# Optimization experiments

Hardware: AMD Instinct MI355X
Metric: run time of the kernel (lower is better)

## Reference

```python
import jax, jax.numpy as jnp
import numpy as np

B = 64        # graphs per batch
N = 2048      # nodes per graph
BN = B * N
BE = BN * 16  # edges (avg degree 16)
C1 = 64
C2 = 64
M = 16
K_EDGES = 4   # hardcoded k=4 in original forward


def setup_inputs() -> dict:
    key = jax.random.key(0)
    k1, k2, k3, k4, k5, k6 = jax.random.split(key, 6)
    x = jax.random.normal(k1, (BN, C1), dtype=jnp.float32)
    e_ = jax.random.randint(k2, (2, BE), 0, BN, dtype=jnp.int32)
    b_ = jnp.repeat(jnp.arange(B, dtype=jnp.int32), N)  # sorted batch index
    # Linear params (stored as (in, out); torch stores (out, in))
    W_assign = jax.random.normal(k3, (C1, M), dtype=jnp.float32) / np.sqrt(C1)
    b_assign = jax.random.normal(k4, (M,), dtype=jnp.float32) * 0.01
    W_embed = jax.random.normal(k5, (C1, C2 - 3), dtype=jnp.float32) / np.sqrt(C1)
    b_embed = jax.random.normal(k6, (C2 - 3,), dtype=jnp.float32) * 0.01
    return {"x": x, "e_": e_, "b_": b_, "W_assign": W_assign,
            "b_assign": b_assign, "W_embed": W_embed, "b_embed": b_embed}


def reference(x, e_, b_, W_assign, b_assign, W_embed, b_embed):
    BN_, _ = x.shape
    Bn = int(jnp.max(b_)) + 1
    Mm = W_assign.shape[1]

    p = x[:, :3]                                   # (BN, 3) positions
    f = x @ W_embed + b_embed                      # (BN, C2-3)
    S = jax.nn.softmax(x @ W_assign + b_assign, axis=-1)  # (BN, M)

    # Weighted scatter-reduce pooling: index_add over (batch*M + m)
    # == per-batch segment_sum of S[n,m] * feat[n,c]
    Zf = jax.ops.segment_sum(S[:, :, None] * f[:, None, :], b_, num_segments=Bn)  # (B, M, C2-3)
    Zp = jax.ops.segment_sum(S[:, :, None] * p[:, None, :], b_, num_segments=Bn)  # (B, M, 3)
    w = jax.ops.segment_sum(S, b_, num_segments=Bn)                               # (B, M)
    w = jnp.maximum(w, 1e-10)
    Zp = Zp / w[..., None]
    x_out = jnp.concatenate([Zp, Zf], axis=-1).reshape(Bn * Mm, -1)  # (B*M, C2)

    # Sparse adjacency pooling: AS = A_NN @ S (A_NN[src,dst]=1 per edge)
    AS = jax.ops.segment_sum(S[e_[1]], e_[0], num_segments=BN_)  # (BN, M)
    # A_MM[b] = (S^T masked to batch b) @ AS
    A_MM = jax.ops.segment_sum(S[:, :, None] * AS[:, None, :], b_, num_segments=Bn)  # (B, M, M)

    # top-k edge construction on pooled adjacency
    dst = jax.lax.top_k(A_MM, K_EDGES)[1]                                # (B, M, k)
    src = jnp.broadcast_to(jnp.arange(Mm)[None, :, None], (Bn, Mm, K_EDGES))
    offset = (jnp.arange(Bn) * Mm)[:, None, None]
    e_out = jnp.stack([(src + offset).reshape(-1), (dst + offset).reshape(-1)], axis=0)
    b_out = jnp.repeat(jnp.arange(Bn), Mm)
    return x_out, e_out, b_out
```

## Files before the change

### kernel.cpp

```cpp
#include <hip/hip_runtime.h>

#define BN 131072
#define BE 2097152
#define NGR 64
#define CAP 36864

#define XS_OFF     0
#define WACC_OFF   262144
#define A_OFF      266240
#define ZERO_U4    20736
#define CUR_OFF    331776
#define QS_OFF     332032
#define ENDS_OFF   333056
#define SH_OFF     2430208
#define PK_OFF     6624512

__global__ __launch_bounds__(256) void k_zero(uint4* __restrict__ zbase,
                                              int* __restrict__ cur)
{
    int zi = blockIdx.x * 256 + threadIdx.x;
    if (zi < ZERO_U4) zbase[zi] = make_uint4(0u, 0u, 0u, 0u);
    if (blockIdx.x == 0 && threadIdx.x < NGR) cur[threadIdx.x] = threadIdx.x * CAP;
}

__global__ __launch_bounds__(256) void k_scatterS(const int* __restrict__ e_,
                                                  int* __restrict__ cur,
                                                  unsigned* __restrict__ packed)
{
    __shared__ int h[64];
    __shared__ int gb[64];
    int t = threadIdx.x;
    if (t < 64) h[t] = 0;
    __syncthreads();
    size_t base = (size_t)blockIdx.x * 4096;
    int e0v[16], e1v[16], rk[16];
    #pragma unroll
    for (int k = 0; k < 16; ++k) {
        size_t i = base + k * 256 + t;
        e0v[k] = e_[i];
        e1v[k] = e_[BE + i];
        rk[k] = atomicAdd(&h[e0v[k] >> 11], 1);
    }
    __syncthreads();
    if (t < 64) gb[t] = atomicAdd(&cur[t], h[t]);
    __syncthreads();
    #pragma unroll
    for (int k = 0; k < 16; ++k) {
        int b = e0v[k] >> 11;
        packed[gb[b] + rk[k]] = ((unsigned)(e0v[k] & 2047) << 17) | (unsigned)e1v[k];
    }
}

__global__ __launch_bounds__(128) void k_node(const float* __restrict__ x,
                                              const float* __restrict__ Wa,
                                              const float* __restrict__ ba,
                                              unsigned short* __restrict__ Sh,
                                              float* __restrict__ Xs,
                                              float* __restrict__ wacc)
{
    __shared__ __align__(16) float Xl[128 * 65];
    __shared__ __align__(16) float Sl[128 * 20];
    __shared__ float Wl[64 * 16];

    const int t = threadIdx.x;
    const int blk = blockIdx.x;
    const int g = blk >> 4;

    const float4* xg4 = (const float4*)(x + (size_t)blk * 128 * 64);
    #pragma unroll
    for (int it = 0; it < 16; ++it) {
        int idx4 = it * 128 + t;
        float4 v = xg4[idx4];
        int node = idx4 >> 4;
        int c4 = (idx4 & 15) * 4;
        float* p = &Xl[node * 65 + c4];
        p[0] = v.x; p[1] = v.y; p[2] = v.z; p[3] = v.w;
    }
    for (int i = t; i < 1024; i += 128) Wl[i] = Wa[i];
    __syncthreads();

    float lg[16];
    #pragma unroll
    for (int m = 0; m < 16; ++m) lg[m] = ba[m];
    for (int c = 0; c < 64; ++c) {
        float xc = Xl[t * 65 + c];
        #pragma unroll
        for (int m = 0; m < 16; ++m) lg[m] += xc * Wl[c * 16 + m];
    }
    float mx = lg[0];
    #pragma unroll
    for (int m = 1; m < 16; ++m) mx = fmaxf(mx, lg[m]);
    float s[16]; float sum = 0.f;
    #pragma unroll
    for (int m = 0; m < 16; ++m) { s[m] = expf(lg[m] - mx); sum += s[m]; }
    float inv = 1.f / sum;
    #pragma unroll
    for (int m = 0; m < 16; ++m) s[m] *= inv;

    const size_t node = (size_t)blk * 128 + t;
    #pragma unroll
    for (int q = 0; q < 4; ++q) {
        float4 v4 = make_float4(s[q*4], s[q*4+1], s[q*4+2], s[q*4+3]);
        *(float4*)(&Sl[t * 20 + q * 4]) = v4;
    }
    {
        unsigned pk8[8];
        #pragma unroll
        for (int j = 0; j < 8; ++j) {
            unsigned b0 = __float_as_uint(s[2*j]);
            unsigned b1 = __float_as_uint(s[2*j+1]);
            unsigned h0 = (b0 + 0x7FFFu + ((b0 >> 16) & 1u)) >> 16;
            unsigned h1 = (b1 + 0x7FFFu + ((b1 >> 16) & 1u)) >> 16;
            pk8[j] = h0 | (h1 << 16);
        }
        uint4* hrow = (uint4*)(Sh + node * 16);
        hrow[0] = make_uint4(pk8[0], pk8[1], pk8[2], pk8[3]);
        hrow[1] = make_uint4(pk8[4], pk8[5], pk8[6], pk8[7]);
    }
    __syncthreads();

    const int c = t & 63;
    const int half = t >> 6;
    float acc[8];
    #pragma unroll
    for (int j = 0; j < 8; ++j) acc[j] = 0.f;
    for (int n = 0; n < 128; ++n) {
        float xv = Xl[n * 65 + c];
        float4 sa = *(const float4*)(&Sl[n * 20 + half * 8]);
        float4 sb = *(const float4*)(&Sl[n * 20 + half * 8 + 4]);
        acc[0] += sa.x * xv; acc[1] += sa.y * xv; acc[2] += sa.z * xv; acc[3] += sa.w * xv;
        acc[4] += sb.x * xv; acc[5] += sb.y * xv; acc[6] += sb.z * xv; acc[7] += sb.w * xv;
    }
    float* xsg = Xs + g * 1024;
    #pragma unroll
    for (int j = 0; j < 8; ++j) atomicAdd(&xsg[(half * 8 + j) * 64 + c], acc[j]);

    if (t < 16) {
        float ws_ = 0.f;
        for (int n = 0; n < 128; ++n) ws_ += Sl[n * 20 + t];
        atomicAdd(&wacc[g * 16 + t], ws_);
    }
}

#define SBUF_CAP 9216
__global__ __launch_bounds__(256) void k_sortL(unsigned* __restrict__ packed,
                                               const int* __restrict__ cur,
                                               int* __restrict__ qs,
                                               int* __restrict__ ends4)
{
    __shared__ unsigned sbuf[SBUF_CAP];
    __shared__ unsigned sout[SBUF_CAP];
    __shared__ int h[2048];
    __shared__ int psum[256];
    const int t = threadIdx.x;
    const int Q = blockIdx.x;
    const int g = Q >> 2;
    const int q = Q & 3;
    const int slab = g * CAP;
    const int n = cur[g] - slab;
    const int chunk = (n + 3) >> 2;
    const int qlo = slab + min(q * chunk, n);
    const int qhi = slab + min((q + 1) * chunk, n);
    const int nq = qhi - qlo;
    if (t == 0) qs[Q] = qlo;

    for (int i = t; i < 2048; i += 256) h[i] = 0;
    __syncthreads();
    for (int i = t; i < nq; i += 256) {
        unsigned u = packed[qlo + i];
        sbuf[i] = u;
        atomicAdd(&h[u >> 17], 1);
    }
    __syncthreads();

    int hl[8]; int s = 0;
    #pragma unroll
    for (int j = 0; j < 8; ++j) { hl[j] = h[t * 8 + j]; s += hl[j]; }
    psum[t] = s;
    __syncthreads();
    for (int off = 1; off < 256; off <<= 1) {
        int v = (t >= off) ? psum[t - off] : 0;
        __syncthreads();
        psum[t] += v;
        __syncthreads();
    }
    int run = psum[t] - s;
    int* ends = ends4 + (Q << 11);
    #pragma unroll
    for (int j = 0; j < 8; ++j) {
        int bin = t * 8 + j;
        int c = hl[j];
        h[bin] = run;
        run += c;
        ends[bin] = qlo + run;
    }
    __syncthreads();
    for (int i = t; i < nq; i += 256) {
        unsigned u = sbuf[i];
        int pos = atomicAdd(&h[u >> 17], 1);
        sout[pos] = u & 131071u;
    }
    __syncthreads();
    for (int i = t; i < nq; i += 256) packed[qlo + i] = sout[i];
}

__global__ __launch_bounds__(256) void k_edge(const unsigned* __restrict__ se1,
                                              const unsigned short* __restrict__ Sh,
                                              const int* __restrict__ ends4,
                                              const int* __restrict__ qs,
                                              float* __restrict__ A)
{
    __shared__ __align__(16) float ASl[64 * 16];
    const int t = threadIdx.x;
    const int blk = blockIdx.x;
    const int g = blk >> 5;
    const int nbase = blk << 6;

    {
        const int qd = t >> 2;
        const int c4 = (t & 3) << 2;
        const int nl = (nbase & 2047) + qd;
        const unsigned short* __restrict__ ShB = Sh + c4;
        float a0 = 0.f, a1 = 0.f, a2 = 0.f, a3 = 0.f;
        float b0 = 0.f, b1 = 0.f, b2 = 0.f, b3 = 0.f;
        #pragma unroll
        for (int q = 0; q < 4; ++q) {
            const int Qb = (g << 2) + q;
            const int* __restrict__ ends = ends4 + (Qb << 11);
            int lo = nl ? ends[nl - 1] : qs[Qb];
            int hi = ends[nl];
            int i = lo;
            for (; i + 2 <= hi; i += 2) {
                unsigned ea = se1[i];
                unsigned eb = se1[i + 1];
                uint2 ra = *(const uint2*)(ShB + ((size_t)ea << 4));
                uint2 rb = *(const uint2*)(ShB + ((size_t)eb << 4));
                a0 += __uint_as_float(ra.x << 16);
                a1 += __uint_as_float(ra.x & 0xFFFF0000u);
                a2 += __uint_as_float(ra.y << 16);
                a3 += __uint_as_float(ra.y & 0xFFFF0000u);
                b0 += __uint_as_float(rb.x << 16);
                b1 += __uint_as_float(rb.x & 0xFFFF0000u);
                b2 += __uint_as_float(rb.y << 16);
                b3 += __uint_as_float(rb.y & 0xFFFF0000u);
            }
            if (i < hi) {
                unsigned ea = se1[i];
                uint2 ra = *(const uint2*)(ShB + ((size_t)ea << 4));
                a0 += __uint_as_float(ra.x << 16);
                a1 += __uint_as_float(ra.x & 0xFFFF0000u);
                a2 += __uint_as_float(ra.y << 16);
                a3 += __uint_as_float(ra.y & 0xFFFF0000u);
            }
        }
        *(float4*)(&ASl[qd * 16 + c4]) = make_float4(a0 + b0, a1 + b1, a2 + b2, a3 + b3);
    }
    __syncthreads();

    {
        const int m = t >> 4;
        const int k = t & 15;
        const unsigned short* __restrict__ SgM = Sh + ((size_t)nbase << 4) + m;
        float a = 0.f;
        #pragma unroll 4
        for (int i = 0; i < 64; ++i) {
            float sv = __uint_as_float((unsigned)SgM[(size_t)i << 4] << 16);
            a += sv * ASl[i * 16 + k];
        }
        atomicAdd(&A[(g << 8) + t], a);
    }
}

__global__ __launch_bounds__(256) void k_xt(const float* __restrict__ Xs,
                                            const float* __restrict__ wacc,
                                            const float* __restrict__ We,
                                            const float* __restrict__ be,
                                            const float* __restrict__ A,
                                            float* __restrict__ out)
{
    const int t = threadIdx.x;
    const int blk = blockIdx.x;
    if (blk < 256) {
        int lane = t & 63;
        int row = blk * 4 + (t >> 6);
        const float* xs = Xs + row * 64;
        float w = wacc[row];
        float val;
        if (lane < 3) {
            val = xs[lane] / fmaxf(w, 1e-10f);
        } else {
            int c2 = lane - 3;
            float accv = w * be[c2];
            for (int cc = 0; cc < 64; ++cc) accv += xs[cc] * We[cc * 61 + c2];
            val = accv;
        }
        out[row * 64 + lane] = val;
    } else {
        int r = (blk - 256) * 256 + t;
        float v[16];
        #pragma unroll
        for (int i = 0; i < 16; ++i) v[i] = A[r * 16 + i];
        float* e0o = out + 65536;
        float* e1o = out + 65536 + 4096;
        float* bo  = out + 65536 + 8192;
        unsigned mask = 0;
        #pragma unroll
        for (int rep = 0; rep < 4; ++rep) {
            float best = -3.4e38f; int bi = 0;
            #pragma unroll
            for (int i = 0; i < 16; ++i) {
                bool ok = (((mask >> i) & 1u) == 0u) && (v[i] > best);
                if (ok) { best = v[i]; bi = i; }
            }
            mask |= (1u << bi);
            e0o[r * 4 + rep] = (float)r;
            e1o[r * 4 + rep] = (float)((r & ~15) + bi);
        }
        bo[r] = (float)(r >> 4);
    }
}

extern "C" void kernel_launch(void* const* d_in, const int* in_sizes, int n_in,
                              void* d_out, int out_size, void* d_ws, size_t ws_size,
                              hipStream_t stream)
{
    const float* x  = (const float*)d_in[0];
    const int*   e  = (const int*)d_in[1];
    const float* Wa = (const float*)d_in[3];
    const float* ba = (const float*)d_in[4];
    const float* We = (const float*)d_in[5];
    const float* be = (const float*)d_in[6];

    char* ws = (char*)d_ws;
    float* Xs     = (float*)(ws + XS_OFF);
    float* wacc   = (float*)(ws + WACC_OFF);
    float* A      = (float*)(ws + A_OFF);
    int*   cur    = (int*)(ws + CUR_OFF);
    int*   qs     = (int*)(ws + QS_OFF);
    int*   ends4  = (int*)(ws + ENDS_OFF);
    unsigned short* Sh = (unsigned short*)(ws + SH_OFF);
    unsigned* packed = (unsigned*)(ws + PK_OFF);

    k_zero    <<<82, 256, 0, stream>>>((uint4*)ws, cur);
    k_scatterS<<<512, 256, 0, stream>>>(e, cur, packed);
    k_node    <<<1024, 128, 0, stream>>>(x, Wa, ba, Sh, Xs, wacc);
    k_sortL   <<<256, 256, 0, stream>>>(packed, cur, qs, ends4);
    k_edge    <<<2048, 256, 0, stream>>>(packed, Sh, ends4, qs, A);
    k_xt      <<<260, 256, 0, stream>>>(Xs, wacc, We, be, A, (float*)d_out);
}
```

Baseline: 104.5 us.

## Fuse edge scatter with node pass and sort with edge aggregation

Edge bucketing and the per-node softmax/pooling kernel are merged into one launch, with block index selecting the role. The local counting sort and the edge gather/A_MM accumulation are also merged, so sorted edge lists stay in shared memory. This removes the global sorted-edge write-back, the ends/qs arrays and two launches. In exchange, all gather work now runs in 256 blocks that loop over 32 node chunks with barriers, instead of 2048 independent blocks, which lowers parallelism for a latency-bound gather.

```diff
diff --git a/kernel.cpp b/kernel.cpp
--- a/kernel.cpp
+++ b/kernel.cpp
@@ -10,10 +10,11 @@
 #define A_OFF      266240
 #define ZERO_U4    20736
 #define CUR_OFF    331776
-#define QS_OFF     332032
-#define ENDS_OFF   333056
-#define SH_OFF     2430208
-#define PK_OFF     6624512
+#define SH_OFF     332032
+#define PK_OFF     4526336
+
+__device__ __forceinline__ float bflo(unsigned u) { return __uint_as_float(u << 16); }
+__device__ __forceinline__ float bfhi(unsigned u) { return __uint_as_float(u & 0xFFFF0000u); }
 
 __global__ __launch_bounds__(256) void k_zero(uint4* __restrict__ zbase,
                                               int* __restrict__ cur)
@@ -23,50 +24,52 @@
     if (blockIdx.x == 0 && threadIdx.x < NGR) cur[threadIdx.x] = threadIdx.x * CAP;
 }
 
-__global__ __launch_bounds__(256) void k_scatterS(const int* __restrict__ e_,
+__global__ __launch_bounds__(128) void k_scatNode(const int* __restrict__ e_,
                                                   int* __restrict__ cur,
-                                                  unsigned* __restrict__ packed)
-{
-    __shared__ int h[64];
-    __shared__ int gb[64];
-    int t = threadIdx.x;
-    if (t < 64) h[t] = 0;
-    __syncthreads();
-    size_t base = (size_t)blockIdx.x * 4096;
-    int e0v[16], e1v[16], rk[16];
-    #pragma unroll
-    for (int k = 0; k < 16; ++k) {
-        size_t i = base + k * 256 + t;
-        e0v[k] = e_[i];
-        e1v[k] = e_[BE + i];
-        rk[k] = atomicAdd(&h[e0v[k] >> 11], 1);
-    }
-    __syncthreads();
-    if (t < 64) gb[t] = atomicAdd(&cur[t], h[t]);
-    __syncthreads();
-    #pragma unroll
-    for (int k = 0; k < 16; ++k) {
-        int b = e0v[k] >> 11;
-        packed[gb[b] + rk[k]] = ((unsigned)(e0v[k] & 2047) << 17) | (unsigned)e1v[k];
-    }
-}
-
-__global__ __launch_bounds__(128) void k_node(const float* __restrict__ x,
-                                              const float* __restrict__ Wa,
-                                              const float* __restrict__ ba,
-                                              unsigned short* __restrict__ Sh,
-                                              float* __restrict__ Xs,
-                                              float* __restrict__ wacc)
-{
-    __shared__ __align__(16) float Xl[128 * 65];
-    __shared__ __align__(16) float Sl[128 * 20];
-    __shared__ float Wl[64 * 16];
-
+                                                  unsigned* __restrict__ packed,
+                                                  const float* __restrict__ x,
+                                                  const float* __restrict__ Wa,
+                                                  const float* __restrict__ ba,
+                                                  unsigned short* __restrict__ Sh,
+                                                  float* __restrict__ Xs,
+                                                  float* __restrict__ wacc)
+{
+    __shared__ __align__(16) unsigned char smem[47616];
     const int t = threadIdx.x;
     const int blk = blockIdx.x;
-    const int g = blk >> 4;
-
-    const float4* xg4 = (const float4*)(x + (size_t)blk * 128 * 64);
+
+    if (blk < 1024) {
+        int* h  = (int*)smem;
+        int* gb = (int*)(smem + 256);
+        if (t < 64) h[t] = 0;
+        __syncthreads();
+        size_t base = (size_t)blk * 2048;
+        int e0v[16], e1v[16], rk[16];
+        #pragma unroll
+        for (int k = 0; k < 16; ++k) {
+            size_t i = base + k * 128 + t;
+            e0v[k] = e_[i];
+            e1v[k] = e_[BE + i];
+            rk[k] = atomicAdd(&h[e0v[k] >> 11], 1);
+        }
+        __syncthreads();
+        if (t < 64) gb[t] = atomicAdd(&cur[t], h[t]);
+        __syncthreads();
+        #pragma unroll
+        for (int k = 0; k < 16; ++k) {
+            int b = e0v[k] >> 11;
+            packed[gb[b] + rk[k]] = ((unsigned)(e0v[k] & 2047) << 17) | (unsigned)e1v[k];
+        }
+        return;
+    }
+
+    const int nblk = blk - 1024;
+    const int g = nblk >> 4;
+    float* Xl = (float*)smem;
+    float* Sl = (float*)(smem + 33280);
+    float* Wl = (float*)(smem + 43520);
+
+    const float4* xg4 = (const float4*)(x + (size_t)nblk * 128 * 64);
     #pragma unroll
     for (int it = 0; it < 16; ++it) {
         int idx4 = it * 128 + t;
@@ -97,7 +100,7 @@
     #pragma unroll
     for (int m = 0; m < 16; ++m) s[m] *= inv;
 
-    const size_t node = (size_t)blk * 128 + t;
+    const size_t node = (size_t)nblk * 128 + t;
     #pragma unroll
     for (int q = 0; q < 4; ++q) {
         float4 v4 = make_float4(s[q*4], s[q*4+1], s[q*4+2], s[q*4+3]);
@@ -142,16 +145,16 @@
     }
 }
 
-#define SBUF_CAP 9216
-__global__ __launch_bounds__(256) void k_sortL(unsigned* __restrict__ packed,
-                                               const int* __restrict__ cur,
-                                               int* __restrict__ qs,
-                                               int* __restrict__ ends4)
-{
-    __shared__ unsigned sbuf[SBUF_CAP];
-    __shared__ unsigned sout[SBUF_CAP];
+#define SE_CAP 9216
+__global__ __launch_bounds__(256) void k_sortEdge(const unsigned* __restrict__ packed,
+                                                  const int* __restrict__ cur,
+                                                  const unsigned short* __restrict__ Sh,
+                                                  float* __restrict__ A)
+{
+    __shared__ unsigned sout[SE_CAP];
     __shared__ int h[2048];
     __shared__ int psum[256];
+    __shared__ __align__(16) float ASl[64 * 16];
     const int t = threadIdx.x;
     const int Q = blockIdx.x;
     const int g = Q >> 2;
@@ -162,13 +165,11 @@
     const int qlo = slab + min(q * chunk, n);
     const int qhi = slab + min((q + 1) * chunk, n);
     const int nq = qhi - qlo;
-    if (t == 0) qs[Q] = qlo;
 
     for (int i = t; i < 2048; i += 256) h[i] = 0;
     __syncthreads();
     for (int i = t; i < nq; i += 256) {
         unsigned u = packed[qlo + i];
-        sbuf[i] = u;
         atomicAdd(&h[u >> 17], 1);
     }
     __syncthreads();
@@ -185,90 +186,60 @@
         __syncthreads();
     }
     int run = psum[t] - s;
-    int* ends = ends4 + (Q << 11);
     #pragma unroll
     for (int j = 0; j < 8; ++j) {
-        int bin = t * 8 + j;
-        int c = hl[j];
-        h[bin] = run;
-        run += c;
-        ends[bin] = qlo + run;
-    }
-    __syncthreads();
+        h[t * 8 + j] = run;
+        run += hl[j];
+    }
+    __syncthreads();
+
     for (int i = t; i < nq; i += 256) {
-        unsigned u = sbuf[i];
+        unsigned u = packed[qlo + i];
         int pos = atomicAdd(&h[u >> 17], 1);
         sout[pos] = u & 131071u;
     }
     __syncthreads();
-    for (int i = t; i < nq; i += 256) packed[qlo + i] = sout[i];
-}
-
-__global__ __launch_bounds__(256) void k_edge(const unsigned* __restrict__ se1,
-                                              const unsigned short* __restrict__ Sh,
-                                              const int* __restrict__ ends4,
-                                              const int* __restrict__ qs,
-                                              float* __restrict__ A)
-{
-    __shared__ __align__(16) float ASl[64 * 16];
-    const int t = threadIdx.x;
-    const int blk = blockIdx.x;
-    const int g = blk >> 5;
-    const int nbase = blk << 6;
-
-    {
-        const int qd = t >> 2;
-        const int c4 = (t & 3) << 2;
-        const int nl = (nbase & 2047) + qd;
-        const unsigned short* __restrict__ ShB = Sh + c4;
+
+    const int qd = t >> 2;
+    const int c4 = (t & 3) << 2;
+    const unsigned short* __restrict__ ShB = Sh + c4;
+    const int m = t >> 4;
+    const int k = t & 15;
+    const unsigned short* __restrict__ SgM = Sh + (((size_t)g << 11) << 4) + m;
+    float aacc = 0.f;
+
+    for (int ch = 0; ch < 32; ++ch) {
+        const int nl = (ch << 6) + qd;
+        int lo = nl ? h[nl - 1] : 0;
+        int hi = h[nl];
         float a0 = 0.f, a1 = 0.f, a2 = 0.f, a3 = 0.f;
         float b0 = 0.f, b1 = 0.f, b2 = 0.f, b3 = 0.f;
-        #pragma unroll
-        for (int q = 0; q < 4; ++q) {
-            const int Qb = (g << 2) + q;
-            const int* __restrict__ ends = ends4 + (Qb << 11);
-            int lo = nl ? ends[nl - 1] : qs[Qb];
-            int hi = ends[nl];
-            int i = lo;
-            for (; i + 2 <= hi; i += 2) {
-                unsigned ea = se1[i];
-                unsigned eb = se1[i + 1];
-                uint2 ra = *(const uint2*)(ShB + ((size_t)ea << 4));
-                uint2 rb = *(const uint2*)(ShB + ((size_t)eb << 4));
-                a0 += __uint_as_float(ra.x << 16);
-                a1 += __uint_as_float(ra.x & 0xFFFF0000u);
-                a2 += __uint_as_float(ra.y << 16);
-                a3 += __uint_as_float(ra.y & 0xFFFF0000u);
-                b0 += __uint_as_float(rb.x << 16);
-                b1 += __uint_as_float(rb.x & 0xFFFF0000u);
-                b2 += __uint_as_float(rb.y << 16);
-                b3 += __uint_as_float(rb.y & 0xFFFF0000u);
-            }
-            if (i < hi) {
-                unsigned ea = se1[i];
-                uint2 ra = *(const uint2*)(ShB + ((size_t)ea << 4));
-                a0 += __uint_as_float(ra.x << 16);
-                a1 += __uint_as_float(ra.x & 0xFFFF0000u);
-                a2 += __uint_as_float(ra.y << 16);
-                a3 += __uint_as_float(ra.y & 0xFFFF0000u);
-            }
+        int i = lo;
+        for (; i + 2 <= hi; i += 2) {
+            unsigned ea = sout[i];
+            unsigned eb = sout[i + 1];
+            uint2 ra = *(const uint2*)(ShB + ((size_t)ea << 4));
+            uint2 rb = *(const uint2*)(ShB + ((size_t)eb << 4));
+            a0 += bflo(ra.x); a1 += bfhi(ra.x); a2 += bflo(ra.y); a3 += bfhi(ra.y);
+            b0 += bflo(rb.x); b1 += bfhi(rb.x); b2 += bflo(rb.y); b3 += bfhi(rb.y);
+        }
+        if (i < hi) {
+            unsigned ea = sout[i];
+            uint2 ra = *(const uint2*)(ShB + ((size_t)ea << 4));
+            a0 += bflo(ra.x); a1 += bfhi(ra.x); a2 += bflo(ra.y); a3 += bfhi(ra.y);
         }
         *(float4*)(&ASl[qd * 16 + c4]) = make_float4(a0 + b0, a1 + b1, a2 + b2, a3 + b3);
-    }
-    __syncthreads();
-
-    {
-        const int m = t >> 4;
-        const int k = t & 15;
-        const unsigned short* __restrict__ SgM = Sh + ((size_t)nbase << 4) + m;
-        float a = 0.f;
+        __syncthreads();
+
+        const int nb = ch << 6;
         #pragma unroll 4
-        for (int i = 0; i < 64; ++i) {
-            float sv = __uint_as_float((unsigned)SgM[(size_t)i << 4] << 16);
-            a += sv * ASl[i * 16 + k];
-        }
-        atomicAdd(&A[(g << 8) + t], a);
-    }
+        for (int i2 = 0; i2 < 64; ++i2) {
+            float sv = __uint_as_float((unsigned)SgM[(size_t)(nb + i2) << 4] << 16);
+            aacc += sv * ASl[i2 * 16 + k];
+        }
+        __syncthreads();
+    }
+    atomicAdd(&A[(g << 8) + t], aacc);
 }
 
 __global__ __launch_bounds__(256) void k_xt(const float* __restrict__ Xs,
@@ -336,15 +307,11 @@
     float* wacc   = (float*)(ws + WACC_OFF);
     float* A      = (float*)(ws + A_OFF);
     int*   cur    = (int*)(ws + CUR_OFF);
-    int*   qs     = (int*)(ws + QS_OFF);
-    int*   ends4  = (int*)(ws + ENDS_OFF);
     unsigned short* Sh = (unsigned short*)(ws + SH_OFF);
     unsigned* packed = (unsigned*)(ws + PK_OFF);
 
     k_zero    <<<82, 256, 0, stream>>>((uint4*)ws, cur);
-    k_scatterS<<<512, 256, 0, stream>>>(e, cur, packed);
-    k_node    <<<1024, 128, 0, stream>>>(x, Wa, ba, Sh, Xs, wacc);
-    k_sortL   <<<256, 256, 0, stream>>>(packed, cur, qs, ends4);
-    k_edge    <<<2048, 256, 0, stream>>>(packed, Sh, ends4, qs, A);
+    k_scatNode<<<2048, 128, 0, stream>>>(e, cur, packed, x, Wa, ba, Sh, Xs, wacc);
+    k_sortEdge<<<256, 256, 0, stream>>>(packed, cur, Sh, A);
     k_xt      <<<260, 256, 0, stream>>>(Xs, wacc, We, be, A, (float*)d_out);
 }
```

Result: slower. 197.0 us (+88.4%).
